# Optimization experiments

Measured on AMD Instinct MI355X. Metric: run time of the kernel, lower is better.

The kernel has to match this reference:

```python
import jax, jax.numpy as jnp
import numpy as np

B, N, D, C = 256, 4096, 128, 32

def setup_inputs() -> dict:
    key = jax.random.key(0)
    k1, k2, k3, k4 = jax.random.split(key, 4)
    queries = jax.random.normal(k1, (B, D), dtype=jnp.float32)
    cases = jax.random.normal(k2, (N, D), dtype=jnp.float32)
    targets = jax.random.normal(k3, (N, C), dtype=jnp.float32)
    feature_weights = jnp.ones((N, D), dtype=jnp.float32)
    distance_weights = jax.random.normal(k4, (N, D), dtype=jnp.float32) * 0.05 - 0.15
    ca_bias = jnp.zeros((N,), dtype=jnp.float32)
    return {
        "queries": queries, "cases": cases, "targets": targets,
        "feature_weights": feature_weights,
        "distance_weights": distance_weights,
        "ca_bias": ca_bias,
    }

def reference(queries, cases, targets, feature_weights, distance_weights, ca_bias):
    # delta: [B, N, D] weighted squared distance per feature
    fw = jax.nn.softplus(feature_weights)                       # [N, D]
    delta = (queries[:, None, :] - cases[None, :, :]) ** 2 * fw[None, :, :]
    # case activations: weighted reduce over D, then sigmoid gate
    w = -jnp.abs(distance_weights)                              # [N, D]
    case_act = jnp.sum(delta * w[None, :, :], axis=2) + ca_bias[None, :]  # [B, N]
    activations = jax.nn.sigmoid(case_act)
    # target adaptation: normalized weighted aggregation of targets
    ca_norm = activations / (jnp.sum(activations, axis=1, keepdims=True) + 0.01)
    y_hat = ca_norm @ targets                                   # [B, C]
    return (y_hat, activations, delta)
```

## Files before the change

### kernel.cpp

```cpp
#include <hip/hip_runtime.h>
#include <math.h>

#define B_ 256
#define N_ 4096
#define D_ 128
#define C_ 32

typedef float vf4 __attribute__((ext_vector_type(4)));

__global__ __launch_bounds__(256) void main_kernel(
    const float* __restrict__ q,
    const float* __restrict__ cases,
    const float* __restrict__ fwin,
    const float* __restrict__ dwin,
    const float* __restrict__ bias,
    float* __restrict__ delta_out,
    float* __restrict__ act_out) {
  const int nc   = blockIdx.x & 255;
  const int bc   = blockIdx.x >> 8;
  const int g    = threadIdx.x >> 5;
  const int lane = threadIdx.x & 31;
  const int d0   = lane * 4;
  const int b0   = bc * 32;

  int   n[2];
  vf4   cv[2], fv[2], wv[2];
  float bn[2];
  n[0] = nc * 16 + g;
  n[1] = n[0] + 8;

  #pragma unroll
  for (int j = 0; j < 2; ++j) {
    const size_t off = (size_t)n[j] * D_ + d0;
    const vf4 x = *(const vf4*)(fwin + off);
    const vf4 w = *(const vf4*)(dwin + off);
    vf4 sp, wvj;
    #pragma unroll
    for (int k = 0; k < 4; ++k) {
      const float xv = x[k];
      sp[k]  = (xv > 20.f) ? xv : log1pf(expf(xv));
      wvj[k] = sp[k] * (-fabsf(w[k]));
    }
    cv[j] = *(const vf4*)(cases + off);
    fv[j] = sp;
    wv[j] = wvj;
    bn[j] = bias[n[j]];
  }

  #pragma unroll 4
  for (int bi = 0; bi < 32; ++bi) {
    const int b = b0 + bi;
    const vf4 qv = *(const vf4*)(q + (size_t)b * D_ + d0);
    #pragma unroll
    for (int j = 0; j < 2; ++j) {
      const vf4 dd = qv - cv[j];
      const vf4 sq = dd * dd;
      const vf4 dl = sq * fv[j];
      __builtin_nontemporal_store(
          dl, (vf4*)(delta_out + ((size_t)b * N_ + n[j]) * D_ + d0));
      const vf4 wa = sq * wv[j];
      float acc = (wa.x + wa.y) + (wa.z + wa.w);
      #pragma unroll
      for (int off = 16; off > 0; off >>= 1)
        acc += __shfl_xor(acc, off, 32);
      const float a = 1.f / (1.f + expf(-(acc + bn[j])));
      if (lane == 0) act_out[(size_t)b * N_ + n[j]] = a;
    }
  }
}

__global__ __launch_bounds__(1024) void finish_kernel(
    const float* __restrict__ act,
    const float* __restrict__ targets,
    float* __restrict__ y) {
  const int b = blockIdx.x;
  const int c = threadIdx.x & 31;
  const int g = threadIdx.x >> 5;
  float ys = 0.f, ss = 0.f;
  for (int n0 = g * 4; n0 < N_; n0 += 128) {
    const vf4 a = *(const vf4*)(act + (size_t)b * N_ + n0);
    ys += a.x * targets[(size_t)(n0 + 0) * C_ + c];
    ys += a.y * targets[(size_t)(n0 + 1) * C_ + c];
    ys += a.z * targets[(size_t)(n0 + 2) * C_ + c];
    ys += a.w * targets[(size_t)(n0 + 3) * C_ + c];
    ss += (a.x + a.y) + (a.z + a.w);
  }
  __shared__ float sm_y[32][33];
  __shared__ float sm_s[32];
  sm_y[g][c] = ys;
  if (c == 0) sm_s[g] = ss;
  __syncthreads();
  if (g == 0) {
    float t = 0.f, s = 0.f;
    #pragma unroll
    for (int k = 0; k < 32; ++k) { t += sm_y[k][c]; s += sm_s[k]; }
    y[(size_t)b * C_ + c] = t / (s + 0.01f);
  }
}

extern "C" void kernel_launch(void* const* d_in, const int* in_sizes, int n_in,
                              void* d_out, int out_size, void* d_ws, size_t ws_size,
                              hipStream_t stream) {
  const float* queries = (const float*)d_in[0];
  const float* cases   = (const float*)d_in[1];
  const float* targets = (const float*)d_in[2];
  const float* fwin    = (const float*)d_in[3];
  const float* dwin    = (const float*)d_in[4];
  const float* bias    = (const float*)d_in[5];

  float* out   = (float*)d_out;
  float* y_hat = out;
  float* act   = out + (size_t)B_ * C_;
  float* delta = act + (size_t)B_ * N_;

  main_kernel<<<2048, 256, 0, stream>>>(queries, cases, fwin, dwin, bias,
                                        delta, act);
  finish_kernel<<<B_, 1024, 0, stream>>>(act, targets, y_hat);
}
```

Baseline: 565.1 us.

## Split activation into expanded-quadratic GEMM-like kernel with precomputed transposed weights

Activation sums are computed through the expansion (q-c)^2*w = q^2*w - 2qc*w + c^2*w. A prep kernel precomputes softplus, transposed weight matrices and a per-case constant, and a dedicated act kernel accumulates q^2*w1 + q*w2 across D without shuffle reductions. The delta kernel now only does the streaming write. This removes the per-element warp shuffle reductions from the bandwidth-bound delta pass, at the cost of an extra prep kernel launch, workspace traffic, and changed floating-point rounding from the expansion.

```diff
diff --git a/kernel.cpp b/kernel.cpp
--- a/kernel.cpp
+++ b/kernel.cpp
@@ -8,14 +8,50 @@
 
 typedef float vf4 __attribute__((ext_vector_type(4)));
 
-__global__ __launch_bounds__(256) void main_kernel(
+__global__ __launch_bounds__(256) void prep_kernel(
+    const float* __restrict__ fwin, const float* __restrict__ dwin,
+    const float* __restrict__ cases, const float* __restrict__ bias,
+    float* __restrict__ fwsp, float* __restrict__ w1t,
+    float* __restrict__ w2t, float* __restrict__ t3) {
+  const int g = threadIdx.x >> 5;
+  const int lane = threadIdx.x & 31;
+  const int n = blockIdx.x * 8 + g;
+  const int d0 = lane * 4;
+  const size_t off = (size_t)n * D_ + d0;
+
+  const vf4 x = *(const vf4*)(fwin + off);
+  const vf4 w = *(const vf4*)(dwin + off);
+  const vf4 c = *(const vf4*)(cases + off);
+
+  vf4 sp, wfw, m2;
+  float s = 0.f;
+  #pragma unroll
+  for (int k = 0; k < 4; ++k) {
+    const float xv = x[k];
+    const float spk = (xv > 20.f) ? xv : log1pf(expf(xv));
+    const float wk = spk * (-fabsf(w[k]));
+    sp[k] = spk;
+    wfw[k] = wk;
+    m2[k] = -2.f * c[k] * wk;
+    s += c[k] * c[k] * wk;
+  }
+  *(vf4*)(fwsp + off) = sp;
+  #pragma unroll
+  for (int k = 0; k < 4; ++k) {
+    w1t[(size_t)(d0 + k) * N_ + n] = wfw[k];
+    w2t[(size_t)(d0 + k) * N_ + n] = m2[k];
+  }
+  #pragma unroll
+  for (int o = 16; o > 0; o >>= 1)
+    s += __shfl_xor(s, o, 32);
+  if (lane == 0) t3[n] = s + bias[n];
+}
+
+__global__ __launch_bounds__(256) void delta_kernel(
     const float* __restrict__ q,
     const float* __restrict__ cases,
-    const float* __restrict__ fwin,
-    const float* __restrict__ dwin,
-    const float* __restrict__ bias,
-    float* __restrict__ delta_out,
-    float* __restrict__ act_out) {
+    const float* __restrict__ fwsp,
+    float* __restrict__ delta_out) {
   const int nc   = blockIdx.x & 255;
   const int bc   = blockIdx.x >> 8;
   const int g    = threadIdx.x >> 5;
@@ -23,28 +59,15 @@
   const int d0   = lane * 4;
   const int b0   = bc * 32;
 
-  int   n[2];
-  vf4   cv[2], fv[2], wv[2];
-  float bn[2];
+  int n[2];
+  vf4 cv[2], fv[2];
   n[0] = nc * 16 + g;
   n[1] = n[0] + 8;
-
   #pragma unroll
   for (int j = 0; j < 2; ++j) {
     const size_t off = (size_t)n[j] * D_ + d0;
-    const vf4 x = *(const vf4*)(fwin + off);
-    const vf4 w = *(const vf4*)(dwin + off);
-    vf4 sp, wvj;
-    #pragma unroll
-    for (int k = 0; k < 4; ++k) {
-      const float xv = x[k];
-      sp[k]  = (xv > 20.f) ? xv : log1pf(expf(xv));
-      wvj[k] = sp[k] * (-fabsf(w[k]));
-    }
     cv[j] = *(const vf4*)(cases + off);
-    fv[j] = sp;
-    wv[j] = wvj;
-    bn[j] = bias[n[j]];
+    fv[j] = *(const vf4*)(fwsp + off);
   }
 
   #pragma unroll 4
@@ -54,17 +77,62 @@
     #pragma unroll
     for (int j = 0; j < 2; ++j) {
       const vf4 dd = qv - cv[j];
-      const vf4 sq = dd * dd;
-      const vf4 dl = sq * fv[j];
+      const vf4 dl = (dd * dd) * fv[j];
       __builtin_nontemporal_store(
           dl, (vf4*)(delta_out + ((size_t)b * N_ + n[j]) * D_ + d0));
-      const vf4 wa = sq * wv[j];
-      float acc = (wa.x + wa.y) + (wa.z + wa.w);
+    }
+  }
+}
+
+__global__ __launch_bounds__(256) void act_kernel(
+    const float* __restrict__ q,
+    const float* __restrict__ w1t,
+    const float* __restrict__ w2t,
+    const float* __restrict__ t3,
+    float* __restrict__ act) {
+  const int bc = blockIdx.x >> 4;
+  const int nc = blockIdx.x & 15;
+  const int kq = threadIdx.x >> 6;
+  const int nl = threadIdx.x & 63;
+  const int n0 = nc * 256 + nl * 4;
+  const int b0 = bc * 8;
+
+  vf4 acc[8];
+  #pragma unroll
+  for (int b = 0; b < 8; ++b) acc[b] = (vf4)(0.f);
+
+  #pragma unroll 4
+  for (int kk = 0; kk < 32; ++kk) {
+    const int k = kq * 32 + kk;
+    const vf4 w1 = *(const vf4*)(w1t + (size_t)k * N_ + n0);
+    const vf4 w2 = *(const vf4*)(w2t + (size_t)k * N_ + n0);
+    #pragma unroll
+    for (int b = 0; b < 8; ++b) {
+      const float a = q[(size_t)(b0 + b) * D_ + k];
+      acc[b] += (a * a) * w1 + a * w2;
+    }
+  }
+
+  __shared__ vf4 part[3][8][64];
+  if (kq > 0) {
+    #pragma unroll
+    for (int b = 0; b < 8; ++b) part[kq - 1][b][nl] = acc[b];
+  }
+  __syncthreads();
+  if (kq == 0) {
+    const vf4 tv = *(const vf4*)(t3 + n0);
+    #pragma unroll
+    for (int t = 0; t < 3; ++t)
       #pragma unroll
-      for (int off = 16; off > 0; off >>= 1)
-        acc += __shfl_xor(acc, off, 32);
-      const float a = 1.f / (1.f + expf(-(acc + bn[j])));
-      if (lane == 0) act_out[(size_t)b * N_ + n[j]] = a;
+      for (int b = 0; b < 8; ++b) acc[b] += part[t][b][nl];
+    #pragma unroll
+    for (int b = 0; b < 8; ++b) {
+      const vf4 ca = acc[b] + tv;
+      vf4 av;
+      #pragma unroll
+      for (int k = 0; k < 4; ++k)
+        av[k] = 1.f / (1.f + __expf(-ca[k]));
+      *(vf4*)(act + (size_t)(b0 + b) * N_ + n0) = av;
     }
   }
 }
@@ -113,7 +181,14 @@
   float* act   = out + (size_t)B_ * C_;
   float* delta = act + (size_t)B_ * N_;
 
-  main_kernel<<<2048, 256, 0, stream>>>(queries, cases, fwin, dwin, bias,
-                                        delta, act);
+  float* fwsp = (float*)d_ws;
+  float* w1t  = fwsp + (size_t)N_ * D_;
+  float* w2t  = w1t + (size_t)D_ * N_;
+  float* t3   = w2t + (size_t)D_ * N_;
+
+  prep_kernel<<<N_ / 8, 256, 0, stream>>>(fwin, dwin, cases, bias,
+                                          fwsp, w1t, w2t, t3);
+  delta_kernel<<<2048, 256, 0, stream>>>(queries, cases, fwsp, delta);
+  act_kernel<<<512, 256, 0, stream>>>(queries, w1t, w2t, t3, act);
   finish_kernel<<<B_, 1024, 0, stream>>>(act, targets, y_hat);
 }
```

New measurement: 581.6 us. 2.9% more time.
